# Performance work log

Hardware: AMD Instinct MI355X
Metric: run time of the kernel (lower is better)

Reference implementation:

```python
import jax, jax.numpy as jnp
import numpy as np

B, T, C = 512, 512, 96


def setup_inputs() -> dict:
    key = jax.random.key(0)
    k1, k2, k3, k4, k5 = jax.random.split(key, 5)
    return {
        "emissions": jax.random.normal(k1, (B, T, C), dtype=jnp.float32),
        "tags": jax.random.randint(k2, (B, T), 0, C, dtype=jnp.int64),
        "mask": jnp.ones((B, T), dtype=bool),
        "start_transitions": jax.random.uniform(k3, (C,), jnp.float32, -0.1, 0.1),
        "end_transitions": jax.random.uniform(k4, (C,), jnp.float32, -0.1, 0.1),
        "transitions": jax.random.uniform(k5, (C, C), jnp.float32, -0.1, 0.1),
    }


def _log_partition(emissions, mask, start_transitions, end_transitions, transitions):
    # alpha: (B, C) forward log-potentials
    alpha0 = start_transitions + emissions[:, 0, :]

    def step(alpha, inp):
        emit_t, mask_t = inp  # (B, C), (B,)
        # scores[b, i, j] = alpha[b, i] + trans[i, j] + emit_t[b, j]
        scores = alpha[:, :, None] + transitions[None, :, :] + emit_t[:, None, :]
        new_alpha = jax.nn.logsumexp(scores, axis=1)  # (B, C)
        alpha = jnp.where(mask_t[:, None], new_alpha, alpha)
        return alpha, None

    emit_seq = jnp.swapaxes(emissions[:, 1:, :], 0, 1)  # (T-1, B, C)
    mask_seq = jnp.swapaxes(mask[:, 1:], 0, 1)          # (T-1, B)
    alpha, _ = jax.lax.scan(step, alpha0, (emit_seq, mask_seq))
    return jax.nn.logsumexp(alpha + end_transitions, axis=1)  # (B,)


def _score(emissions, tags, mask, start_transitions, end_transitions, transitions):
    maskf = mask.astype(emissions.dtype)
    # emission score at the gold tag each step: (B, T)
    emit = jnp.take_along_axis(emissions, tags[:, :, None], axis=2)[:, :, 0]
    trans = transitions[tags[:, :-1], tags[:, 1:]]  # (B, T-1)
    score = start_transitions[tags[:, 0]] + emit[:, 0]
    score = score + jnp.sum((emit[:, 1:] + trans) * maskf[:, 1:], axis=1)
    lengths = mask.astype(jnp.int32).sum(axis=1)
    last_tag = jnp.take_along_axis(tags, (lengths - 1)[:, None], axis=1)[:, 0]
    return score + end_transitions[last_tag]


def reference(emissions, tags, mask, start_transitions, end_transitions, transitions):
    log_den = _log_partition(emissions, mask, start_transitions, end_transitions, transitions)
    log_num = _score(emissions, tags, mask, start_transitions, end_transitions, transitions)
    return jnp.mean(log_den - log_num)
```

## Files before the change

kernel.cpp:

```cpp
#include <hip/hip_runtime.h>


#define CB 512
#define CT 512
#define CC 96
#define L2E 1.4426950408889634f
#define LN2 0.6931471805599453f

typedef __attribute__((ext_vector_type(2))) float f32x2;
typedef __attribute__((ext_vector_type(4))) float f32x4;

#define PK_FMA_LO(acc, e2, p2) \
    asm("v_pk_fma_f32 %0, %1, %2, %0 op_sel_hi:[1,0,1]" : "+v"(acc) : "v"(e2), "v"(p2))
#define PK_FMA_HI(acc, e2, p2) \
    asm("v_pk_fma_f32 %0, %1, %2, %0 op_sel:[0,1,0]" : "+v"(acc) : "v"(e2), "v"(p2))

__global__ __launch_bounds__(64, 1) void crf_fwd_kernel(
    const float* __restrict__ emissions,
    const int*   __restrict__ tags,
    const float* __restrict__ start_t,
    const float* __restrict__ end_t,
    const float* __restrict__ trans,
    float* __restrict__ out)
{
    const int l = threadIdx.x;
    const int b = blockIdx.x;
    const bool hi = (l < 32);
    const int jb = hi ? (64 + l) : (CC - 1);

    __shared__ __align__(16) float pbuf[128];

    const float* em = emissions + (size_t)b * CT * CC;

    float pfa0 = em[1 * CC + l],  pfa1 = em[2 * CC + l],
          pfa2 = em[3 * CC + l],  pfa3 = em[4 * CC + l];
    float pfb0 = em[1 * CC + jb], pfb1 = em[2 * CC + jb],
          pfb2 = em[3 * CC + jb], pfb3 = em[4 * CC + jb];
    float ea0 = em[0 * CC + l];
    float eb0 = em[0 * CC + jb];

    f32x2 E2[CC];
#pragma unroll
    for (int i = 0; i < CC; ++i) {
        E2[i].x = __builtin_amdgcn_exp2f(trans[i * CC + l]  * L2E);
        E2[i].y = __builtin_amdgcn_exp2f(trans[i * CC + jb] * L2E);
    }

    float za = (start_t[l]  + ea0) * L2E;
    float zb = (start_t[jb] + eb0) * L2E;
    float ref0 = __int_as_float(__builtin_amdgcn_readlane(__float_as_int(za), 0));
    const float base2f = ref0;
    int   S = 0;
    float scale = 1.0f;
    pbuf[l]      = __builtin_amdgcn_exp2f(za - ref0);
    pbuf[64 + l] = __builtin_amdgcn_exp2f(zb - ref0);
    __builtin_amdgcn_wave_barrier();

    const f32x4* p4 = (const f32x4*)pbuf;
    const float* pa = em + 5 * CC + l;
    const float* pb = em + 5 * CC + jb;
    f32x2 q;

#define STEP(SLOTA, SLOTB, DO_LOAD, LOADOFF)                                  \
    {                                                                         \
        f32x2 x2;                                                             \
        x2.x = __builtin_amdgcn_exp2f(SLOTA * L2E) * scale;                   \
        x2.y = __builtin_amdgcn_exp2f(SLOTB * L2E) * scale;                   \
        if (DO_LOAD) { SLOTA = pa[LOADOFF]; SLOTB = pb[LOADOFF]; }            \
        f32x2 ac0 = {0.f, 0.f}, ac1 = {0.f, 0.f};                             \
        f32x2 ac2 = {0.f, 0.f}, ac3 = {0.f, 0.f};                             \
        _Pragma("unroll")                                                     \
        for (int u = 0; u < CC / 4; ++u) {                                    \
            f32x4 pv = p4[u];                                                 \
            f32x2 plo = __builtin_shufflevector(pv, pv, 0, 1);                \
            f32x2 phi = __builtin_shufflevector(pv, pv, 2, 3);                \
            PK_FMA_LO(ac0, E2[4 * u + 0], plo);                               \
            PK_FMA_HI(ac1, E2[4 * u + 1], plo);                               \
            PK_FMA_LO(ac2, E2[4 * u + 2], phi);                               \
            PK_FMA_HI(ac3, E2[4 * u + 3], phi);                               \
        }                                                                     \
        q = ((ac0 + ac1) + (ac2 + ac3)) * x2;                                 \
        pbuf[l]      = q.x;     \
        pbuf[64 + l] = q.y;                                                   \
        __builtin_amdgcn_wave_barrier();                                      \
        unsigned ru = (unsigned)__builtin_amdgcn_readlane(                    \
                          __float_as_int(q.x), 0);                            \
        int ebits = (int)(ru >> 23) & 0xff;                                   \
        S += ebits - 127;                                                     \
        scale = __uint_as_float((unsigned)(254 - ebits) << 23);               \
    }

    for (int k = 0; k < 126; ++k) {
        STEP(pfa0, pfb0, 1, 0 * CC)
        STEP(pfa1, pfb1, 1, 1 * CC)
        STEP(pfa2, pfb2, 1, 2 * CC)
        STEP(pfa3, pfb3, 1, 3 * CC)
        pa += 4 * CC;
        pb += 4 * CC;
    }
    STEP(pfa0, pfb0, 1, 0 * CC)
    STEP(pfa1, pfb1, 1, 1 * CC)
    STEP(pfa2, pfb2, 1, 2 * CC)
    STEP(pfa3, pfb3, 0, 0)
    STEP(pfa0, pfb0, 0, 0)
    STEP(pfa1, pfb1, 0, 0)
    STEP(pfa2, pfb2, 0, 0)
#undef STEP

    float v = q.x * scale * __builtin_amdgcn_exp2f(end_t[l] * L2E);
    if (hi) v += q.y * scale * __builtin_amdgcn_exp2f(end_t[jb] * L2E);
#pragma unroll
    for (int off = 32; off; off >>= 1) v += __shfl_down(v, off);
    float den = 0.f;
    if (l == 0) den = LN2 * (base2f + (float)S + __builtin_amdgcn_logf(v));

    const int* tg = tags + b * CT;
    float sc = 0.f;
    for (int t = l; t < CT; t += 64) {
        int c = tg[t];
        float e = em[t * CC + c];
        if (t == 0) sc += start_t[c] + e;
        else        sc += e + trans[tg[t - 1] * CC + c];
        if (t == CT - 1) sc += end_t[c];
    }
#pragma unroll
    for (int off = 32; off; off >>= 1) sc += __shfl_down(sc, off);

    if (l == 0) atomicAdd(out, (den - sc) * (1.0f / CB));
}

extern "C" void kernel_launch(void* const* d_in, const int* in_sizes, int n_in,
                              void* d_out, int out_size, void* d_ws, size_t ws_size,
                              hipStream_t stream) {
    const float* emissions = (const float*)d_in[0];
    const int*   tags      = (const int*)d_in[1];
    const float* start_t   = (const float*)d_in[3];
    const float* end_t     = (const float*)d_in[4];
    const float* trans     = (const float*)d_in[5];
    float* out = (float*)d_out;

    hipMemsetAsync(out, 0, sizeof(float), stream);
    crf_fwd_kernel<<<CB, 64, 0, stream>>>(emissions, tags, start_t, end_t, trans, out);
}
```

Before: 393.4 us.

## Process two batch sequences per wave with 48 active lanes over column pairs

Each 64-lane wave now runs two batch elements at once. Lanes own adjacent column pairs (48 lanes cover the 96 tags), and the exp(transition) registers are shared between both sequences. The grid shrinks to 256 blocks, which gives two independent dependency chains per step for latency hiding, but halves the number of waves and leaves 16 lanes idle. The prefetch depth drops from 4 steps to 3.

```diff
diff --git a/kernel.cpp b/kernel.cpp
--- a/kernel.cpp
+++ b/kernel.cpp
@@ -24,109 +24,165 @@
     float* __restrict__ out)
 {
     const int l = threadIdx.x;
-    const int b = blockIdx.x;
-    const bool hi = (l < 32);
-    const int jb = hi ? (64 + l) : (CC - 1);
-
-    __shared__ __align__(16) float pbuf[128];
-
-    const float* em = emissions + (size_t)b * CT * CC;
-
-    float pfa0 = em[1 * CC + l],  pfa1 = em[2 * CC + l],
-          pfa2 = em[3 * CC + l],  pfa3 = em[4 * CC + l];
-    float pfb0 = em[1 * CC + jb], pfb1 = em[2 * CC + jb],
-          pfb2 = em[3 * CC + jb], pfb3 = em[4 * CC + jb];
-    float ea0 = em[0 * CC + l];
-    float eb0 = em[0 * CC + jb];
+    const int bA = blockIdx.x * 2;
+    const int bB = bA + 1;
+    const int lc  = (l < 48) ? l : 47;
+    const int col = 2 * lc;
+
+    __shared__ __align__(16) float pbufA[CC];
+    __shared__ __align__(16) float pbufB[CC];
+
+    const float* emA = emissions + (size_t)bA * CT * CC;
+    const float* emB = emissions + (size_t)bB * CT * CC;
 
     f32x2 E2[CC];
 #pragma unroll
     for (int i = 0; i < CC; ++i) {
-        E2[i].x = __builtin_amdgcn_exp2f(trans[i * CC + l]  * L2E);
-        E2[i].y = __builtin_amdgcn_exp2f(trans[i * CC + jb] * L2E);
-    }
-
-    float za = (start_t[l]  + ea0) * L2E;
-    float zb = (start_t[jb] + eb0) * L2E;
-    float ref0 = __int_as_float(__builtin_amdgcn_readlane(__float_as_int(za), 0));
-    const float base2f = ref0;
-    int   S = 0;
-    float scale = 1.0f;
-    pbuf[l]      = __builtin_amdgcn_exp2f(za - ref0);
-    pbuf[64 + l] = __builtin_amdgcn_exp2f(zb - ref0);
+        f32x2 tr = *(const f32x2*)(trans + i * CC + col);
+        E2[i].x = __builtin_amdgcn_exp2f(tr.x * L2E);
+        E2[i].y = __builtin_amdgcn_exp2f(tr.y * L2E);
+    }
+
+    f32x2 st = *(const f32x2*)(start_t + col);
+    f32x2 e0A = *(const f32x2*)(emA + col);
+    f32x2 e0B = *(const f32x2*)(emB + col);
+    f32x2 zA, zB;
+    zA.x = (st.x + e0A.x) * L2E;  zA.y = (st.y + e0A.y) * L2E;
+    zB.x = (st.x + e0B.x) * L2E;  zB.y = (st.y + e0B.y) * L2E;
+    const float refA = __int_as_float(__builtin_amdgcn_readlane(__float_as_int(zA.x), 0));
+    const float refB = __int_as_float(__builtin_amdgcn_readlane(__float_as_int(zB.x), 0));
+    int   SAi = 0, SBi = 0;
+    float scaleA = 1.0f, scaleB = 1.0f;
+    f32x2 w;
+    w.x = __builtin_amdgcn_exp2f(zA.x - refA);
+    w.y = __builtin_amdgcn_exp2f(zA.y - refA);
+    ((f32x2*)pbufA)[lc] = w;
+    w.x = __builtin_amdgcn_exp2f(zB.x - refB);
+    w.y = __builtin_amdgcn_exp2f(zB.y - refB);
+    ((f32x2*)pbufB)[lc] = w;
     __builtin_amdgcn_wave_barrier();
 
-    const f32x4* p4 = (const f32x4*)pbuf;
-    const float* pa = em + 5 * CC + l;
-    const float* pb = em + 5 * CC + jb;
-    f32x2 q;
-
-#define STEP(SLOTA, SLOTB, DO_LOAD, LOADOFF)                                  \
+    f32x2 sA0 = *(const f32x2*)(emA + 1 * CC + col);
+    f32x2 sA1 = *(const f32x2*)(emA + 2 * CC + col);
+    f32x2 sA2 = *(const f32x2*)(emA + 3 * CC + col);
+    f32x2 sB0 = *(const f32x2*)(emB + 1 * CC + col);
+    f32x2 sB1 = *(const f32x2*)(emB + 2 * CC + col);
+    f32x2 sB2 = *(const f32x2*)(emB + 3 * CC + col);
+    const float* paA = emA + 4 * CC + col;
+    const float* paB = emB + 4 * CC + col;
+
+    const f32x4* p4A = (const f32x4*)pbufA;
+    const f32x4* p4B = (const f32x4*)pbufB;
+    f32x2 qA, qB;
+
+#define STEP(SA, SB, DO_LOAD, LOADOFF)                                        \
     {                                                                         \
-        f32x2 x2;                                                             \
-        x2.x = __builtin_amdgcn_exp2f(SLOTA * L2E) * scale;                   \
-        x2.y = __builtin_amdgcn_exp2f(SLOTB * L2E) * scale;                   \
-        if (DO_LOAD) { SLOTA = pa[LOADOFF]; SLOTB = pb[LOADOFF]; }            \
-        f32x2 ac0 = {0.f, 0.f}, ac1 = {0.f, 0.f};                             \
-        f32x2 ac2 = {0.f, 0.f}, ac3 = {0.f, 0.f};                             \
+        f32x2 xA, xB;                                                         \
+        xA.x = __builtin_amdgcn_exp2f(SA.x * L2E) * scaleA;                   \
+        xA.y = __builtin_amdgcn_exp2f(SA.y * L2E) * scaleA;                   \
+        xB.x = __builtin_amdgcn_exp2f(SB.x * L2E) * scaleB;                   \
+        xB.y = __builtin_amdgcn_exp2f(SB.y * L2E) * scaleB;                   \
+        if (DO_LOAD) {                                                        \
+            SA = *(const f32x2*)(paA + (LOADOFF));                            \
+            SB = *(const f32x2*)(paB + (LOADOFF));                            \
+        }                                                                     \
+        f32x2 aA0 = {0.f,0.f}, aA1 = {0.f,0.f}, aA2 = {0.f,0.f}, aA3 = {0.f,0.f}; \
+        f32x2 aB0 = {0.f,0.f}, aB1 = {0.f,0.f}, aB2 = {0.f,0.f}, aB3 = {0.f,0.f}; \
         _Pragma("unroll")                                                     \
         for (int u = 0; u < CC / 4; ++u) {                                    \
-            f32x4 pv = p4[u];                                                 \
+            f32x4 pv = p4A[u];                                                \
             f32x2 plo = __builtin_shufflevector(pv, pv, 0, 1);                \
             f32x2 phi = __builtin_shufflevector(pv, pv, 2, 3);                \
-            PK_FMA_LO(ac0, E2[4 * u + 0], plo);                               \
-            PK_FMA_HI(ac1, E2[4 * u + 1], plo);                               \
-            PK_FMA_LO(ac2, E2[4 * u + 2], phi);                               \
-            PK_FMA_HI(ac3, E2[4 * u + 3], phi);                               \
+            PK_FMA_LO(aA0, E2[4 * u + 0], plo);                               \
+            PK_FMA_HI(aA1, E2[4 * u + 1], plo);                               \
+            PK_FMA_LO(aA2, E2[4 * u + 2], phi);                               \
+            PK_FMA_HI(aA3, E2[4 * u + 3], phi);                               \
         }                                                                     \
-        q = ((ac0 + ac1) + (ac2 + ac3)) * x2;                                 \
-        pbuf[l]      = q.x;     \
-        pbuf[64 + l] = q.y;                                                   \
+        _Pragma("unroll")                                                     \
+        for (int u = 0; u < CC / 4; ++u) {                                    \
+            f32x4 pv = p4B[u];                                                \
+            f32x2 plo = __builtin_shufflevector(pv, pv, 0, 1);                \
+            f32x2 phi = __builtin_shufflevector(pv, pv, 2, 3);                \
+            PK_FMA_LO(aB0, E2[4 * u + 0], plo);                               \
+            PK_FMA_HI(aB1, E2[4 * u + 1], plo);                               \
+            PK_FMA_LO(aB2, E2[4 * u + 2], phi);                               \
+            PK_FMA_HI(aB3, E2[4 * u + 3], phi);                               \
+        }                                                                     \
+        qA = ((aA0 + aA1) + (aA2 + aA3)) * xA;                                \
+        qB = ((aB0 + aB1) + (aB2 + aB3)) * xB;                                \
+        ((f32x2*)pbufA)[lc] = qA;                                             \
+        ((f32x2*)pbufB)[lc] = qB;                                             \
         __builtin_amdgcn_wave_barrier();                                      \
-        unsigned ru = (unsigned)__builtin_amdgcn_readlane(                    \
-                          __float_as_int(q.x), 0);                            \
-        int ebits = (int)(ru >> 23) & 0xff;                                   \
-        S += ebits - 127;                                                     \
-        scale = __uint_as_float((unsigned)(254 - ebits) << 23);               \
-    }
-
-    for (int k = 0; k < 126; ++k) {
-        STEP(pfa0, pfb0, 1, 0 * CC)
-        STEP(pfa1, pfb1, 1, 1 * CC)
-        STEP(pfa2, pfb2, 1, 2 * CC)
-        STEP(pfa3, pfb3, 1, 3 * CC)
-        pa += 4 * CC;
-        pb += 4 * CC;
-    }
-    STEP(pfa0, pfb0, 1, 0 * CC)
-    STEP(pfa1, pfb1, 1, 1 * CC)
-    STEP(pfa2, pfb2, 1, 2 * CC)
-    STEP(pfa3, pfb3, 0, 0)
-    STEP(pfa0, pfb0, 0, 0)
-    STEP(pfa1, pfb1, 0, 0)
-    STEP(pfa2, pfb2, 0, 0)
+        unsigned ruA = (unsigned)__builtin_amdgcn_readlane(__float_as_int(qA.x), 0); \
+        int ebA = (int)(ruA >> 23) & 0xff;                                    \
+        SAi += ebA - 127;                                                     \
+        scaleA = __uint_as_float((unsigned)(254 - ebA) << 23);                \
+        unsigned ruB = (unsigned)__builtin_amdgcn_readlane(__float_as_int(qB.x), 0); \
+        int ebB = (int)(ruB >> 23) & 0xff;                                    \
+        SBi += ebB - 127;                                                     \
+        scaleB = __uint_as_float((unsigned)(254 - ebB) << 23);                \
+    }
+
+    for (int k = 0; k < 169; ++k) {
+        STEP(sA0, sB0, 1, 0 * CC)
+        STEP(sA1, sB1, 1, 1 * CC)
+        STEP(sA2, sB2, 1, 2 * CC)
+        paA += 3 * CC;
+        paB += 3 * CC;
+    }
+    STEP(sA0, sB0, 1, 0)
+    STEP(sA1, sB1, 0, 0)
+    STEP(sA2, sB2, 0, 0)
+    STEP(sA0, sB0, 0, 0)
 #undef STEP
 
-    float v = q.x * scale * __builtin_amdgcn_exp2f(end_t[l] * L2E);
-    if (hi) v += q.y * scale * __builtin_amdgcn_exp2f(end_t[jb] * L2E);
+    f32x2 en = *(const f32x2*)(end_t + col);
+    float vA = 0.f, vB = 0.f;
+    if (l < 48) {
+        float fx = __builtin_amdgcn_exp2f(en.x * L2E);
+        float fy = __builtin_amdgcn_exp2f(en.y * L2E);
+        vA = qA.x * scaleA * fx + qA.y * scaleA * fy;
+        vB = qB.x * scaleB * fx + qB.y * scaleB * fy;
+    }
 #pragma unroll
-    for (int off = 32; off; off >>= 1) v += __shfl_down(v, off);
-    float den = 0.f;
-    if (l == 0) den = LN2 * (base2f + (float)S + __builtin_amdgcn_logf(v));
-
-    const int* tg = tags + b * CT;
-    float sc = 0.f;
+    for (int off = 32; off; off >>= 1) {
+        vA += __shfl_down(vA, off);
+        vB += __shfl_down(vB, off);
+    }
+    float denA = 0.f, denB = 0.f;
+    if (l == 0) {
+        denA = LN2 * (refA + (float)SAi + __builtin_amdgcn_logf(vA));
+        denB = LN2 * (refB + (float)SBi + __builtin_amdgcn_logf(vB));
+    }
+
+    const int* tgA = tags + bA * CT;
+    const int* tgB = tags + bB * CT;
+    float scA = 0.f, scB = 0.f;
     for (int t = l; t < CT; t += 64) {
-        int c = tg[t];
-        float e = em[t * CC + c];
-        if (t == 0) sc += start_t[c] + e;
-        else        sc += e + trans[tg[t - 1] * CC + c];
-        if (t == CT - 1) sc += end_t[c];
+        int cA = tgA[t];
+        int cB = tgB[t];
+        float eA_ = emA[t * CC + cA];
+        float eB_ = emB[t * CC + cB];
+        if (t == 0) {
+            scA += start_t[cA] + eA_;
+            scB += start_t[cB] + eB_;
+        } else {
+            scA += eA_ + trans[tgA[t - 1] * CC + cA];
+            scB += eB_ + trans[tgB[t - 1] * CC + cB];
+        }
+        if (t == CT - 1) {
+            scA += end_t[cA];
+            scB += end_t[cB];
+        }
     }
 #pragma unroll
-    for (int off = 32; off; off >>= 1) sc += __shfl_down(sc, off);
-
-    if (l == 0) atomicAdd(out, (den - sc) * (1.0f / CB));
+    for (int off = 32; off; off >>= 1) {
+        scA += __shfl_down(scA, off);
+        scB += __shfl_down(scB, off);
+    }
+
+    if (l == 0)
+        atomicAdd(out, ((denA - scA) + (denB - scB)) * (1.0f / CB));
 }
 
 extern "C" void kernel_launch(void* const* d_in, const int* in_sizes, int n_in,
@@ -140,5 +196,5 @@
     float* out = (float*)d_out;
 
     hipMemsetAsync(out, 0, sizeof(float), stream);
-    crf_fwd_kernel<<<CB, 64, 0, stream>>>(emissions, tags, start_t, end_t, trans, out);
+    crf_fwd_kernel<<<CB / 2, 64, 0, stream>>>(emissions, tags, start_t, end_t, trans, out);
 }
```

New measurement: 652.0 us. 1.66x slower.

## Broadcast alpha via SGPR readlane instead of LDS round-trip each step

Applied to the files above, without the earlier changes.

Each lane now owns two adjacent tag columns (48 active lanes), and the previous step's probabilities are broadcast with readlane into SGPR pairs feeding packed FMAs, replacing the LDS store/barrier/vector-load exchange. This removes LDS latency from the serial time-step dependency chain. In exchange each step issues 96 readlanes on the scalar path, which can serialize on the VALU-to-SGPR hazards, and 16 lanes sit idle.

```diff
diff --git a/kernel.cpp b/kernel.cpp
--- a/kernel.cpp
+++ b/kernel.cpp
@@ -8,12 +8,13 @@
 #define LN2 0.6931471805599453f
 
 typedef __attribute__((ext_vector_type(2))) float f32x2;
-typedef __attribute__((ext_vector_type(4))) float f32x4;
 
-#define PK_FMA_LO(acc, e2, p2) \
-    asm("v_pk_fma_f32 %0, %1, %2, %0 op_sel_hi:[1,0,1]" : "+v"(acc) : "v"(e2), "v"(p2))
-#define PK_FMA_HI(acc, e2, p2) \
-    asm("v_pk_fma_f32 %0, %1, %2, %0 op_sel:[0,1,0]" : "+v"(acc) : "v"(e2), "v"(p2))
+#define PK_FMA(acc, ex, p64) \
+    asm("v_pk_fma_f32 %0, %1, %2, %0" : "+v"(acc) : "v"(ex), "s"(p64))
+
+__device__ __forceinline__ float rl(float v, int lane) {
+    return __int_as_float(__builtin_amdgcn_readlane(__float_as_int(v), lane));
+}
 
 __global__ __launch_bounds__(64, 1) void crf_fwd_kernel(
     const float* __restrict__ emissions,
@@ -25,64 +26,68 @@
 {
     const int l = threadIdx.x;
     const int b = blockIdx.x;
-    const bool hi = (l < 32);
-    const int jb = hi ? (64 + l) : (CC - 1);
-
-    __shared__ __align__(16) float pbuf[128];
+    const int lc  = (l < 48) ? l : 47;
+    const int col = 2 * lc;
 
     const float* em = emissions + (size_t)b * CT * CC;
 
-    float pfa0 = em[1 * CC + l],  pfa1 = em[2 * CC + l],
-          pfa2 = em[3 * CC + l],  pfa3 = em[4 * CC + l];
-    float pfb0 = em[1 * CC + jb], pfb1 = em[2 * CC + jb],
-          pfb2 = em[3 * CC + jb], pfb3 = em[4 * CC + jb];
-    float ea0 = em[0 * CC + l];
-    float eb0 = em[0 * CC + jb];
-
-    f32x2 E2[CC];
+    f32x2 EX[CC / 2], EY[CC / 2];
 #pragma unroll
-    for (int i = 0; i < CC; ++i) {
-        E2[i].x = __builtin_amdgcn_exp2f(trans[i * CC + l]  * L2E);
-        E2[i].y = __builtin_amdgcn_exp2f(trans[i * CC + jb] * L2E);
+    for (int k = 0; k < CC / 2; ++k) {
+        f32x2 t0 = *(const f32x2*)(trans + (2 * k)     * CC + col);
+        f32x2 t1 = *(const f32x2*)(trans + (2 * k + 1) * CC + col);
+        EX[k].x = __builtin_amdgcn_exp2f(t0.x * L2E);
+        EX[k].y = __builtin_amdgcn_exp2f(t1.x * L2E);
+        EY[k].x = __builtin_amdgcn_exp2f(t0.y * L2E);
+        EY[k].y = __builtin_amdgcn_exp2f(t1.y * L2E);
     }
 
-    float za = (start_t[l]  + ea0) * L2E;
-    float zb = (start_t[jb] + eb0) * L2E;
-    float ref0 = __int_as_float(__builtin_amdgcn_readlane(__float_as_int(za), 0));
-    const float base2f = ref0;
+    f32x2 st = *(const f32x2*)(start_t + col);
+    f32x2 e0 = *(const f32x2*)(em + col);
+    float zx = (st.x + e0.x) * L2E;
+    float zy = (st.y + e0.y) * L2E;
+    const float ref0 = rl(zx, 0);
     int   S = 0;
     float scale = 1.0f;
-    pbuf[l]      = __builtin_amdgcn_exp2f(za - ref0);
-    pbuf[64 + l] = __builtin_amdgcn_exp2f(zb - ref0);
-    __builtin_amdgcn_wave_barrier();
+    f32x2 q;
+    q.x = __builtin_amdgcn_exp2f(zx - ref0);
+    q.y = __builtin_amdgcn_exp2f(zy - ref0);
 
-    const f32x4* p4 = (const f32x4*)pbuf;
-    const float* pa = em + 5 * CC + l;
-    const float* pb = em + 5 * CC + jb;
-    f32x2 q;
+    f32x2 s0 = *(const f32x2*)(em + 1 * CC + col);
+    f32x2 s1 = *(const f32x2*)(em + 2 * CC + col);
+    f32x2 s2 = *(const f32x2*)(em + 3 * CC + col);
+    f32x2 s3 = *(const f32x2*)(em + 4 * CC + col);
+    const float* pa = em + 5 * CC + col;
 
-#define STEP(SLOTA, SLOTB, DO_LOAD, LOADOFF)                                  \
+#define STEP(SLOT, DO_LOAD, LOADOFF)                                          \
     {                                                                         \
         f32x2 x2;                                                             \
-        x2.x = __builtin_amdgcn_exp2f(SLOTA * L2E) * scale;                   \
-        x2.y = __builtin_amdgcn_exp2f(SLOTB * L2E) * scale;                   \
-        if (DO_LOAD) { SLOTA = pa[LOADOFF]; SLOTB = pb[LOADOFF]; }            \
-        f32x2 ac0 = {0.f, 0.f}, ac1 = {0.f, 0.f};                             \
-        f32x2 ac2 = {0.f, 0.f}, ac3 = {0.f, 0.f};                             \
+        x2.x = __builtin_amdgcn_exp2f(SLOT.x * L2E) * scale;                  \
+        x2.y = __builtin_amdgcn_exp2f(SLOT.y * L2E) * scale;                  \
+        if (DO_LOAD) SLOT = *(const f32x2*)(pa + (LOADOFF));                  \
+        f32x2 aX0 = {0.f, 0.f}, aX1 = {0.f, 0.f};                             \
+        f32x2 aY0 = {0.f, 0.f}, aY1 = {0.f, 0.f};                             \
         _Pragma("unroll")                                                     \
-        for (int u = 0; u < CC / 4; ++u) {                                    \
-            f32x4 pv = p4[u];                                                 \
-            f32x2 plo = __builtin_shufflevector(pv, pv, 0, 1);                \
-            f32x2 phi = __builtin_shufflevector(pv, pv, 2, 3);                \
-            PK_FMA_LO(ac0, E2[4 * u + 0], plo);                               \
-            PK_FMA_HI(ac1, E2[4 * u + 1], plo);                               \
-            PK_FMA_LO(ac2, E2[4 * u + 2], phi);                               \
-            PK_FMA_HI(ac3, E2[4 * u + 3], phi);                               \
+        for (int k = 0; k < CC / 2; k += 2) {                                 \
+            unsigned lo0 = (unsigned)__builtin_amdgcn_readlane(               \
+                               __float_as_int(q.x), k);                       \
+            unsigned hi0 = (unsigned)__builtin_amdgcn_readlane(               \
+                               __float_as_int(q.y), k);                       \
+            long long p0 = (long long)(((unsigned long long)hi0 << 32) | lo0);\
+            PK_FMA(aX0, EX[k], p0);                                           \
+            PK_FMA(aY0, EY[k], p0);                                           \
+            unsigned lo1 = (unsigned)__builtin_amdgcn_readlane(               \
+                               __float_as_int(q.x), k + 1);                   \
+            unsigned hi1 = (unsigned)__builtin_amdgcn_readlane(               \
+                               __float_as_int(q.y), k + 1);                   \
+            long long p1 = (long long)(((unsigned long long)hi1 << 32) | lo1);\
+            PK_FMA(aX1, EX[k + 1], p1);                                       \
+            PK_FMA(aY1, EY[k + 1], p1);                                       \
         }                                                                     \
-        q = ((ac0 + ac1) + (ac2 + ac3)) * x2;                                 \
-        pbuf[l]      = q.x;     \
-        pbuf[64 + l] = q.y;                                                   \
-        __builtin_amdgcn_wave_barrier();                                      \
+        f32x2 aX = aX0 + aX1;                                                 \
+        f32x2 aY = aY0 + aY1;                                                 \
+        q.x = (aX.x + aX.y) * x2.x;                                           \
+        q.y = (aY.x + aY.y) * x2.y;                                           \
         unsigned ru = (unsigned)__builtin_amdgcn_readlane(                    \
                           __float_as_int(q.x), 0);                            \
         int ebits = (int)(ru >> 23) & 0xff;                                   \
@@ -91,28 +96,31 @@
     }
 
     for (int k = 0; k < 126; ++k) {
-        STEP(pfa0, pfb0, 1, 0 * CC)
-        STEP(pfa1, pfb1, 1, 1 * CC)
-        STEP(pfa2, pfb2, 1, 2 * CC)
-        STEP(pfa3, pfb3, 1, 3 * CC)
+        STEP(s0, 1, 0 * CC)
+        STEP(s1, 1, 1 * CC)
+        STEP(s2, 1, 2 * CC)
+        STEP(s3, 1, 3 * CC)
         pa += 4 * CC;
-        pb += 4 * CC;
     }
-    STEP(pfa0, pfb0, 1, 0 * CC)
-    STEP(pfa1, pfb1, 1, 1 * CC)
-    STEP(pfa2, pfb2, 1, 2 * CC)
-    STEP(pfa3, pfb3, 0, 0)
-    STEP(pfa0, pfb0, 0, 0)
-    STEP(pfa1, pfb1, 0, 0)
-    STEP(pfa2, pfb2, 0, 0)
+    STEP(s0, 1, 0 * CC)
+    STEP(s1, 1, 1 * CC)
+    STEP(s2, 1, 2 * CC)
+    STEP(s3, 0, 0)
+    STEP(s0, 0, 0)
+    STEP(s1, 0, 0)
+    STEP(s2, 0, 0)
 #undef STEP
 
-    float v = q.x * scale * __builtin_amdgcn_exp2f(end_t[l] * L2E);
-    if (hi) v += q.y * scale * __builtin_amdgcn_exp2f(end_t[jb] * L2E);
+    f32x2 en = *(const f32x2*)(end_t + col);
+    float v = 0.f;
+    if (l < 48) {
+        v = q.x * scale * __builtin_amdgcn_exp2f(en.x * L2E)
+          + q.y * scale * __builtin_amdgcn_exp2f(en.y * L2E);
+    }
 #pragma unroll
     for (int off = 32; off; off >>= 1) v += __shfl_down(v, off);
     float den = 0.f;
-    if (l == 0) den = LN2 * (base2f + (float)S + __builtin_amdgcn_logf(v));
+    if (l == 0) den = LN2 * (ref0 + (float)S + __builtin_amdgcn_logf(v));
 
     const int* tg = tags + b * CT;
     float sc = 0.f;
```

Measured after the change: 338.2 us. -14.0%, faster.
